# Kernel optimization log

Measured on AMD Instinct MI355X. Metric: run time of the kernel, lower is better.

## Reference

```python
import jax, jax.numpy as jnp
import numpy as np

EPS = 1e-5


def _batchnorm(x, gamma, beta):
    # training-mode batch norm over the node axis, per feature channel
    mean = jnp.mean(x, axis=0)
    var = jnp.var(x, axis=0)  # biased variance, as torch uses for normalization
    return (x - mean) * jax.lax.rsqrt(var + EPS) * gamma + beta


def _gcn_conv(h, W, b, src, dst, norm, n_nodes):
    # h: [N, Fin] -> [N, Fout]; D^{-1/2}(A+I)D^{-1/2} (h W) + b
    h = h @ W                                   # [N, Fout]
    msgs = h[src] * norm[:, None]               # [E+N, Fout] gathered, normalized
    out = jax.ops.segment_sum(msgs, dst, num_segments=n_nodes)
    return out + b


def setup_inputs() -> dict:
    key = jax.random.key(0)
    ks = jax.random.split(key, 8)
    N, F, E, H = 50000, 512, 800000, 256
    inp = {
        "x": jax.random.normal(ks[0], (N, F), jnp.float32),
        "edge_index": jax.random.randint(ks[1], (2, E), 0, N, jnp.int64),
        "gamma1": jnp.ones((F,), jnp.float32),
        "beta1": jnp.zeros((F,), jnp.float32),
        "W1": jax.random.normal(ks[2], (F, H), jnp.float32) * (1.0 / np.sqrt(F)),
        "b1": jnp.zeros((H,), jnp.float32),
        "W2": jax.random.normal(ks[3], (H, H), jnp.float32) * (1.0 / np.sqrt(H)),
        "b2": jnp.zeros((H,), jnp.float32),
        "W3": jax.random.normal(ks[4], (H, H), jnp.float32) * (1.0 / np.sqrt(H)),
        "b3": jnp.zeros((H,), jnp.float32),
        "W4": jax.random.normal(ks[5], (H, H), jnp.float32) * (1.0 / np.sqrt(H)),
        "b4": jnp.zeros((H,), jnp.float32),
        "gamma2": jnp.ones((H,), jnp.float32),
        "beta2": jnp.zeros((H,), jnp.float32),
        "Wd": jax.random.normal(ks[6], (H, 5), jnp.float32) * (1.0 / np.sqrt(H)),
        "bd": jnp.zeros((5,), jnp.float32),
    }
    return inp


def reference(x, edge_index, gamma1, beta1, W1, b1, W2, b2, W3, b3, W4, b4,
              gamma2, beta2, Wd, bd):
    N = x.shape[0]
    loops = jnp.arange(N, dtype=edge_index.dtype)
    src = jnp.concatenate([edge_index[0], loops])
    dst = jnp.concatenate([edge_index[1], loops])
    deg = jax.ops.segment_sum(jnp.ones_like(src, dtype=x.dtype), dst, num_segments=N)
    dinv = jax.lax.rsqrt(deg)                    # deg >= 1 due to self-loops
    norm = dinv[src] * dinv[dst]                 # [E+N]

    h = _batchnorm(x, gamma1, beta1)
    h = _gcn_conv(h, W1, b1, src, dst, norm, N)
    h = _gcn_conv(h, W2, b2, src, dst, norm, N)
    h = _gcn_conv(h, W3, b3, src, dst, norm, N)
    h = _gcn_conv(h, W4, b4, src, dst, norm, N)
    h = _batchnorm(h, gamma2, beta2)
    # Flatten(start_dim=1) is identity on [N, 256]
    return jax.nn.sigmoid(h @ Wd + bd)           # [N, 5]
```

## Files before the change

kernel.cpp:

```cpp
#include <hip/hip_runtime.h>
#include <math.h>

#define BN_EPS 1e-5f

typedef float floatx4 __attribute__((ext_vector_type(4)));
typedef short shortx4 __attribute__((ext_vector_type(4)));
typedef short shortx8 __attribute__((ext_vector_type(8)));
typedef __bf16 bf16x8 __attribute__((ext_vector_type(8)));

__device__ __forceinline__ unsigned short f2b(float f) {
    unsigned int u = __builtin_bit_cast(unsigned int, f);
    u += 0x7fffu + ((u >> 16) & 1u);
    return (unsigned short)(u >> 16);
}
__device__ __forceinline__ float b2f(unsigned short s) {
    unsigned int u = ((unsigned int)s) << 16;
    return __builtin_bit_cast(float, u);
}
__device__ __forceinline__ float b2f_s(short s) { return b2f((unsigned short)s); }

__global__ __launch_bounds__(256)
void k_detect(const unsigned int* __restrict__ ei, int n_check, int* __restrict__ flag) {
    __shared__ int any;
    if (threadIdx.x == 0) any = 0;
    __syncthreads();
    for (int i = threadIdx.x; i < n_check; i += 256) {
        if (ei[2 * i + 1] != 0u) any = 1;
    }
    __syncthreads();
    if (threadIdx.x == 0) *flag = any;
}

__global__ __launch_bounds__(256)
void k_convert(const void* __restrict__ ei_raw, const int* __restrict__ flag,
               int* __restrict__ src, int* __restrict__ dst, int E) {
    int e = blockIdx.x * 256 + threadIdx.x;
    if (e >= E) return;
    if (*flag) {
        const int* a = (const int*)ei_raw;
        src[e] = a[e];
        dst[e] = a[E + e];
    } else {
        const long long* a = (const long long*)ei_raw;
        src[e] = (int)a[e];
        dst[e] = (int)a[E + e];
    }
}

__global__ __launch_bounds__(256)
void k_count(const int* __restrict__ dst, int* __restrict__ cnt, int E) {
    int e = blockIdx.x * 256 + threadIdx.x;
    if (e < E) atomicAdd(&cnt[dst[e]], 1);
}

__global__ __launch_bounds__(1024)
void k_scan_sum(const int* __restrict__ cnt, int* __restrict__ bsum, int N) {
    __shared__ int s[1024];
    int i = blockIdx.x * 1024 + threadIdx.x;
    s[threadIdx.x] = (i < N) ? cnt[i] : 0;
    __syncthreads();
    for (int off = 512; off > 0; off >>= 1) {
        if (threadIdx.x < off) s[threadIdx.x] += s[threadIdx.x + off];
        __syncthreads();
    }
    if (threadIdx.x == 0) bsum[blockIdx.x] = s[0];
}

__global__ __launch_bounds__(1024)
void k_scan_part(int* __restrict__ bsum, int nb) {
    __shared__ int s[1024];
    int t = threadIdx.x;
    int v = (t < nb) ? bsum[t] : 0;
    s[t] = v;
    __syncthreads();
    for (int off = 1; off < 1024; off <<= 1) {
        int tmp = (t >= off) ? s[t - off] : 0;
        __syncthreads();
        s[t] += tmp;
        __syncthreads();
    }
    if (t < nb) bsum[t] = s[t] - v;
}

__global__ __launch_bounds__(1024)
void k_scan_final(const int* __restrict__ cnt, const int* __restrict__ bsum,
                  int* __restrict__ row_ptr, int* __restrict__ cursor,
                  float* __restrict__ dinv, int N) {
    __shared__ int s[1024];
    int b = blockIdx.x, t = threadIdx.x;
    int i = b * 1024 + t;
    int v = (i < N) ? cnt[i] : 0;
    s[t] = v;
    __syncthreads();
    for (int off = 1; off < 1024; off <<= 1) {
        int tmp = (t >= off) ? s[t - off] : 0;
        __syncthreads();
        s[t] += tmp;
        __syncthreads();
    }
    if (i < N) {
        int excl = bsum[b] + s[t] - v;
        row_ptr[i] = excl;
        cursor[i]  = excl;
        dinv[i] = rsqrtf((float)(v + 1));
        if (i == N - 1) row_ptr[N] = excl + v;
    }
}

__global__ __launch_bounds__(256)
void k_fill(const int* __restrict__ src, const int* __restrict__ dst,
            int* __restrict__ cursor, const float* __restrict__ dinv,
            int2* __restrict__ csr_sw, int E) {
    int e = blockIdx.x * 256 + threadIdx.x;
    if (e >= E) return;
    int s = src[e], d = dst[e];
    int p = atomicAdd(&cursor[d], 1);
    float w = dinv[s] * dinv[d];
    csr_sw[p] = make_int2(s, __builtin_bit_cast(int, w));
}

__global__ __launch_bounds__(256)
void k_bnstats(const float* __restrict__ x, float* __restrict__ sum, float* __restrict__ sumsq,
               int N, int F) {
    __shared__ float ls[512], lq[512];
    int q   = F >> 2;
    int t   = threadIdx.x;
    int cq  = t % q;
    int ro  = t / q;
    int rpp = 256 / q;
    int step = gridDim.x * rpp;
    float s0 = 0.f, s1 = 0.f, s2 = 0.f, s3 = 0.f;
    float q0 = 0.f, q1 = 0.f, q2 = 0.f, q3 = 0.f;
    for (int r = blockIdx.x * rpp + ro; r < N; r += 2 * step) {
        float4 v = *(const float4*)&x[(size_t)r * F + cq * 4];
        int r2 = r + step;
        if (r2 < N) {
            float4 u = *(const float4*)&x[(size_t)r2 * F + cq * 4];
            s0 += u.x; s1 += u.y; s2 += u.z; s3 += u.w;
            q0 += u.x * u.x; q1 += u.y * u.y; q2 += u.z * u.z; q3 += u.w * u.w;
        }
        s0 += v.x; s1 += v.y; s2 += v.z; s3 += v.w;
        q0 += v.x * v.x; q1 += v.y * v.y; q2 += v.z * v.z; q3 += v.w * v.w;
    }
    for (int c = t; c < F; c += 256) { ls[c] = 0.f; lq[c] = 0.f; }
    __syncthreads();
    atomicAdd(&ls[cq * 4 + 0], s0); atomicAdd(&ls[cq * 4 + 1], s1);
    atomicAdd(&ls[cq * 4 + 2], s2); atomicAdd(&ls[cq * 4 + 3], s3);
    atomicAdd(&lq[cq * 4 + 0], q0); atomicAdd(&lq[cq * 4 + 1], q1);
    atomicAdd(&lq[cq * 4 + 2], q2); atomicAdd(&lq[cq * 4 + 3], q3);
    __syncthreads();
    for (int c = t; c < F; c += 256) {
        atomicAdd(&sum[c],   ls[c]);
        atomicAdd(&sumsq[c], lq[c]);
    }
}

__global__ __launch_bounds__(256)
void k_bnstats_b(const unsigned short* __restrict__ x, float* __restrict__ sum,
                 float* __restrict__ sumsq, int N, int H) {
    __shared__ float ls[256], lq[256];
    int t  = threadIdx.x;
    int cg = t & 31;
    int ro = t >> 5;
    int step = gridDim.x * 8;
    float s[8], q[8];
    #pragma unroll
    for (int j = 0; j < 8; ++j) { s[j] = 0.f; q[j] = 0.f; }
    for (int r = blockIdx.x * 8 + ro; r < N; r += step) {
        shortx8 v = *(const shortx8*)&x[(size_t)r * H + cg * 8];
        #pragma unroll
        for (int j = 0; j < 8; ++j) {
            float f = b2f_s(v[j]);
            s[j] += f; q[j] += f * f;
        }
    }
    ls[t] = 0.f; lq[t] = 0.f;
    __syncthreads();
    #pragma unroll
    for (int j = 0; j < 8; ++j) {
        atomicAdd(&ls[cg * 8 + j], s[j]);
        atomicAdd(&lq[cg * 8 + j], q[j]);
    }
    __syncthreads();
    atomicAdd(&sum[t],   ls[t]);
    atomicAdd(&sumsq[t], lq[t]);
}

__global__ __launch_bounds__(256)
void k_bnfin(const float* __restrict__ sum, const float* __restrict__ sumsq,
             const float* __restrict__ gamma, const float* __restrict__ beta,
             float* __restrict__ a, float* __restrict__ b, int N, int F) {
    int c = blockIdx.x * 256 + threadIdx.x;
    if (c >= F) return;
    float m   = sum[c] / (float)N;
    float var = sumsq[c] / (float)N - m * m;
    float rs  = rsqrtf(var + BN_EPS);
    float aa  = gamma[c] * rs;
    a[c] = aa;
    b[c] = beta[c] - m * aa;
}

__global__ __launch_bounds__(256)
void k_cast_bn(const float* __restrict__ x, const float* __restrict__ a, const float* __restrict__ b,
               unsigned short* __restrict__ xb, int N, int F, int Mpad) {
    int i = blockIdx.x * 256 + threadIdx.x;
    int total = Mpad * (F / 8);
    if (i >= total) return;
    int row = i / (F / 8);
    int col = (i % (F / 8)) * 8;
    shortx8 v;
    if (row < N) {
        float4 x0 = *(const float4*)&x[(size_t)row * F + col];
        float4 x1 = *(const float4*)&x[(size_t)row * F + col + 4];
        float4 a0 = *(const float4*)&a[col];
        float4 a1 = *(const float4*)&a[col + 4];
        float4 b0 = *(const float4*)&b[col];
        float4 b1 = *(const float4*)&b[col + 4];
        v[0] = (short)f2b(x0.x * a0.x + b0.x);
        v[1] = (short)f2b(x0.y * a0.y + b0.y);
        v[2] = (short)f2b(x0.z * a0.z + b0.z);
        v[3] = (short)f2b(x0.w * a0.w + b0.w);
        v[4] = (short)f2b(x1.x * a1.x + b1.x);
        v[5] = (short)f2b(x1.y * a1.y + b1.y);
        v[6] = (short)f2b(x1.z * a1.z + b1.z);
        v[7] = (short)f2b(x1.w * a1.w + b1.w);
    } else {
        #pragma unroll
        for (int j = 0; j < 8; ++j) v[j] = 0;
    }
    *(shortx8*)&xb[(size_t)row * F + col] = v;
}

__global__ __launch_bounds__(256)
void k_castWT4(const float* __restrict__ W1, const float* __restrict__ W2,
               const float* __restrict__ W3, const float* __restrict__ W4,
               unsigned short* __restrict__ T1, unsigned short* __restrict__ T2,
               unsigned short* __restrict__ T3, unsigned short* __restrict__ T4,
               int F, int H) {
    int i = blockIdx.x * 256 + threadIdx.x;
    int n1 = F * H, n2 = H * H;
    const float* W; unsigned short* T; int K; int j;
    if (i < n1)               { W = W1; T = T1; K = F; j = i; }
    else if (i < n1 + n2)     { W = W2; T = T2; K = H; j = i - n1; }
    else if (i < n1 + 2 * n2) { W = W3; T = T3; K = H; j = i - n1 - n2; }
    else if (i < n1 + 3 * n2) { W = W4; T = T4; K = H; j = i - n1 - 2 * n2; }
    else return;
    int n = j / K, k = j % K;
    T[j] = f2b(W[(size_t)k * H + n]);
}

__device__ __forceinline__ void glds16(const void* g, void* l) {
    __builtin_amdgcn_global_load_lds(
        (const __attribute__((address_space(1))) unsigned int*)g,
        (__attribute__((address_space(3))) unsigned int*)l, 16, 0, 0);
}

__global__ __launch_bounds__(256)
void k_gemm_bf16(const unsigned short* __restrict__ A, const unsigned short* __restrict__ Bt,
                 unsigned short* __restrict__ C, int K, int NC) {
    __shared__ unsigned short As[128 * 32];
    __shared__ unsigned short Bs[128 * 32];
    int tid  = threadIdx.x;
    int wave = tid >> 6, lane = tid & 63;
    int row0 = blockIdx.x * 128;
    int col0 = blockIdx.y * 128;
    int wr = (wave & 1) * 64;
    int wc = (wave >> 1) * 64;

    floatx4 acc[4][4];
    #pragma unroll
    for (int i = 0; i < 4; i++)
        #pragma unroll
        for (int j = 0; j < 4; j++) acc[i][j] = (floatx4){0.f, 0.f, 0.f, 0.f};

    int cA = tid * 16;
    int cB = cA + 4096;
    const char* Ab = (const char*)A;
    const char* Bb = (const char*)Bt;
    size_t a_off0 = (size_t)(row0 + (cA >> 6)) * K * 2 + (cA & 63);
    size_t a_off1 = (size_t)(row0 + (cB >> 6)) * K * 2 + (cB & 63);
    size_t b_off0 = (size_t)(col0 + (cA >> 6)) * K * 2 + (cA & 63);
    size_t b_off1 = (size_t)(col0 + (cB >> 6)) * K * 2 + (cB & 63);

    int lm  = lane & 15;
    int lk8 = (lane >> 4) * 8;

    for (int ks = 0; ks < K; ks += 32) {
        size_t koff = (size_t)ks * 2;
        glds16(Ab + a_off0 + koff, (char*)As + cA);
        glds16(Ab + a_off1 + koff, (char*)As + cA + 4096);
        glds16(Bb + b_off0 + koff, (char*)Bs + cA);
        glds16(Bb + b_off1 + koff, (char*)Bs + cA + 4096);
        __syncthreads();

        bf16x8 af[4], bfr[4];
        #pragma unroll
        for (int i = 0; i < 4; i++) {
            shortx8 s = *(const shortx8*)&As[(wr + i * 16 + lm) * 32 + lk8];
            af[i] = __builtin_bit_cast(bf16x8, s);
        }
        #pragma unroll
        for (int j = 0; j < 4; j++) {
            shortx8 s = *(const shortx8*)&Bs[(wc + j * 16 + lm) * 32 + lk8];
            bfr[j] = __builtin_bit_cast(bf16x8, s);
        }
        #pragma unroll
        for (int i = 0; i < 4; i++)
            #pragma unroll
            for (int j = 0; j < 4; j++)
                acc[i][j] = __builtin_amdgcn_mfma_f32_16x16x32_bf16(af[i], bfr[j], acc[i][j], 0, 0, 0);
        __syncthreads();
    }

    int crow = row0 + wr + (lane >> 4) * 4;
    int ccol = col0 + wc + lm;
    #pragma unroll
    for (int i = 0; i < 4; i++)
        #pragma unroll
        for (int j = 0; j < 4; j++)
            #pragma unroll
            for (int r = 0; r < 4; r++)
                C[(size_t)(crow + i * 16 + r) * NC + ccol + j * 16] = f2b(acc[i][j][r]);
}

__global__ __launch_bounds__(256)
void k_agg(const unsigned short* __restrict__ hin, unsigned short* __restrict__ hout,
           const int* __restrict__ row_ptr, const int2* __restrict__ csr_sw,
           const float* __restrict__ dinv, const float* __restrict__ bias, int N) {
    const int H = 256;
    int node = blockIdx.x * 4 + (threadIdx.x >> 6);
    if (node >= N) return;
    int lane = threadIdx.x & 63;
    int half = lane >> 5;
    int f = (lane & 31) * 8;
    float acc[8];
    float di = dinv[node];
    if (half == 0) {
        shortx8 hv = *(const shortx8*)&hin[(size_t)node * H + f];
        float sl = di * di;
        #pragma unroll
        for (int j = 0; j < 8; ++j) acc[j] = b2f_s(hv[j]) * sl;
    } else {
        #pragma unroll
        for (int j = 0; j < 8; ++j) acc[j] = 0.f;
    }
    int e0 = row_ptr[node], e1 = row_ptr[node + 1];
    int e = e0;
    for (; e + 8 <= e1; e += 8) {
        int2 p0 = csr_sw[e + 0 + half];
        int2 p1 = csr_sw[e + 2 + half];
        int2 p2 = csr_sw[e + 4 + half];
        int2 p3 = csr_sw[e + 6 + half];
        shortx8 r0 = *(const shortx8*)&hin[(size_t)p0.x * H + f];
        shortx8 r1 = *(const shortx8*)&hin[(size_t)p1.x * H + f];
        shortx8 r2 = *(const shortx8*)&hin[(size_t)p2.x * H + f];
        shortx8 r3 = *(const shortx8*)&hin[(size_t)p3.x * H + f];
        float w0 = __builtin_bit_cast(float, p0.y);
        float w1 = __builtin_bit_cast(float, p1.y);
        float w2 = __builtin_bit_cast(float, p2.y);
        float w3 = __builtin_bit_cast(float, p3.y);
        #pragma unroll
        for (int j = 0; j < 8; ++j)
            acc[j] += w0 * b2f_s(r0[j]) + w1 * b2f_s(r1[j])
                    + w2 * b2f_s(r2[j]) + w3 * b2f_s(r3[j]);
    }
    for (; e < e1; e += 2) {
        int idx = e + half;
        bool valid = idx < e1;
        int2 pr = csr_sw[valid ? idx : e];
        float w = valid ? __builtin_bit_cast(float, pr.y) : 0.f;
        shortx8 r = *(const shortx8*)&hin[(size_t)pr.x * H + f];
        #pragma unroll
        for (int j = 0; j < 8; ++j) acc[j] += w * b2f_s(r[j]);
    }
    #pragma unroll
    for (int j = 0; j < 8; ++j) acc[j] += __shfl_xor(acc[j], 32, 64);
    if (half == 0) {
        float4 bi0 = *(const float4*)&bias[f];
        float4 bi1 = *(const float4*)&bias[f + 4];
        shortx8 o;
        o[0] = (short)f2b(acc[0] + bi0.x);
        o[1] = (short)f2b(acc[1] + bi0.y);
        o[2] = (short)f2b(acc[2] + bi0.z);
        o[3] = (short)f2b(acc[3] + bi0.w);
        o[4] = (short)f2b(acc[4] + bi1.x);
        o[5] = (short)f2b(acc[5] + bi1.y);
        o[6] = (short)f2b(acc[6] + bi1.z);
        o[7] = (short)f2b(acc[7] + bi1.w);
        *(shortx8*)&hout[(size_t)node * H + f] = o;
    }
}

__global__ __launch_bounds__(256)
void k_head(const unsigned short* __restrict__ h, const float* __restrict__ a,
            const float* __restrict__ b, const float* __restrict__ Wd,
            const float* __restrict__ bd, float* __restrict__ out, int N) {
    int node = blockIdx.x * 4 + (threadIdx.x >> 6);
    if (node >= N) return;
    int lane = threadIdx.x & 63;
    int f = lane * 4;
    shortx4 hv = *(const shortx4*)&h[(size_t)node * 256 + f];
    float v0 = b2f_s(hv[0]) * a[f + 0] + b[f + 0];
    float v1 = b2f_s(hv[1]) * a[f + 1] + b[f + 1];
    float v2 = b2f_s(hv[2]) * a[f + 2] + b[f + 2];
    float v3 = b2f_s(hv[3]) * a[f + 3] + b[f + 3];
    float s[5];
    #pragma unroll
    for (int j = 0; j < 5; ++j) {
        s[j] = v0 * Wd[(f + 0) * 5 + j] + v1 * Wd[(f + 1) * 5 + j] +
               v2 * Wd[(f + 2) * 5 + j] + v3 * Wd[(f + 3) * 5 + j];
    }
    #pragma unroll
    for (int off = 32; off > 0; off >>= 1) {
        #pragma unroll
        for (int j = 0; j < 5; ++j) s[j] += __shfl_down(s[j], off, 64);
    }
    if (lane == 0) {
        #pragma unroll
        for (int j = 0; j < 5; ++j) {
            float z = s[j] + bd[j];
            out[(size_t)node * 5 + j] = 1.f / (1.f + expf(-z));
        }
    }
}

extern "C" void kernel_launch(void* const* d_in, const int* in_sizes, int n_in,
                              void* d_out, int out_size, void* d_ws, size_t ws_size,
                              hipStream_t stream) {
    const float* x      = (const float*)d_in[0];
    const void*  ei_raw = d_in[1];
    const float* gamma1 = (const float*)d_in[2];
    const float* beta1  = (const float*)d_in[3];
    const float* W1 = (const float*)d_in[4];
    const float* b1 = (const float*)d_in[5];
    const float* W2 = (const float*)d_in[6];
    const float* b2 = (const float*)d_in[7];
    const float* W3 = (const float*)d_in[8];
    const float* b3 = (const float*)d_in[9];
    const float* W4 = (const float*)d_in[10];
    const float* b4 = (const float*)d_in[11];
    const float* gamma2 = (const float*)d_in[12];
    const float* beta2  = (const float*)d_in[13];
    const float* Wd = (const float*)d_in[14];
    const float* bd = (const float*)d_in[15];

    const int F = in_sizes[2];
    const int N = in_sizes[0] / F;
    const int E = in_sizes[1] / 2;
    const int H = in_sizes[5];
    const int Mpad = ((N + 127) / 128) * 128;
    const int NB   = (N + 1023) / 1024;
    float* out = (float*)d_out;

    char* p = (char*)d_ws;
    auto alloc = [&](size_t bytes) {
        void* r = (void*)p;
        p += (bytes + 255) & ~(size_t)255;
        return r;
    };
    int*   flag    = (int*)  alloc(4);
    int*   srcA    = (int*)  alloc((size_t)E * 4);
    int*   dstA    = (int*)  alloc((size_t)E * 4);
    int*   cnt     = (int*)  alloc((size_t)N * 4);
    int*   row_ptr = (int*)  alloc(((size_t)N + 1) * 4);
    int*   cursor  = (int*)  alloc((size_t)N * 4);
    float* dinv    = (float*)alloc((size_t)N * 4);
    int2*  csr_sw  = (int2*) alloc((size_t)E * 8);
    int*   bsum    = (int*)  alloc((size_t)NB * 4);
    float* colsum  = (float*)alloc((size_t)F * 4);
    float* colsq   = (float*)alloc((size_t)F * 4);
    float* bna     = (float*)alloc((size_t)F * 4);
    float* bnb     = (float*)alloc((size_t)F * 4);
    unsigned short* W1t = (unsigned short*)alloc((size_t)F * H * 2);
    unsigned short* W2t = (unsigned short*)alloc((size_t)H * H * 2);
    unsigned short* W3t = (unsigned short*)alloc((size_t)H * H * 2);
    unsigned short* W4t = (unsigned short*)alloc((size_t)H * H * 2);
    unsigned short* xb  = (unsigned short*)alloc((size_t)Mpad * F * 2);
    unsigned short* hbA = (unsigned short*)alloc((size_t)Mpad * H * 2);
    unsigned short* hbB = (unsigned short*)alloc((size_t)Mpad * H * 2);

    hipMemsetAsync(cnt,    0, (size_t)N * 4, stream);
    hipMemsetAsync(colsum, 0, (size_t)F * 4, stream);
    hipMemsetAsync(colsq,  0, (size_t)F * 4, stream);

    int n_check = (E >= 2048) ? 2048 : E;
    k_detect<<<1, 256, 0, stream>>>((const unsigned int*)ei_raw, n_check, flag);
    k_convert<<<(E + 255) / 256, 256, 0, stream>>>(ei_raw, flag, srcA, dstA, E);
    k_count<<<(E + 255) / 256, 256, 0, stream>>>(dstA, cnt, E);
    k_scan_sum<<<NB, 1024, 0, stream>>>(cnt, bsum, N);
    k_scan_part<<<1, 1024, 0, stream>>>(bsum, NB);
    k_scan_final<<<NB, 1024, 0, stream>>>(cnt, bsum, row_ptr, cursor, dinv, N);
    k_fill<<<(E + 255) / 256, 256, 0, stream>>>(srcA, dstA, cursor, dinv, csr_sw, E);

    k_bnstats<<<1024, 256, 0, stream>>>(x, colsum, colsq, N, F);
    k_bnfin<<<(F + 255) / 256, 256, 0, stream>>>(colsum, colsq, gamma1, beta1, bna, bnb, N, F);
    k_cast_bn<<<(Mpad * (F / 8) + 255) / 256, 256, 0, stream>>>(x, bna, bnb, xb, N, F, Mpad);

    int tot = F * H + 3 * H * H;
    k_castWT4<<<(tot + 255) / 256, 256, 0, stream>>>(W1, W2, W3, W4, W1t, W2t, W3t, W4t, F, H);

    dim3 gg(Mpad / 128, H / 128);
    int aggb = (N + 3) / 4;
    k_gemm_bf16<<<gg, 256, 0, stream>>>(xb, W1t, hbA, F, H);
    k_agg<<<aggb, 256, 0, stream>>>(hbA, hbB, row_ptr, csr_sw, dinv, b1, N);
    k_gemm_bf16<<<gg, 256, 0, stream>>>(hbB, W2t, hbA, H, H);
    k_agg<<<aggb, 256, 0, stream>>>(hbA, hbB, row_ptr, csr_sw, dinv, b2, N);
    k_gemm_bf16<<<gg, 256, 0, stream>>>(hbB, W3t, hbA, H, H);
    k_agg<<<aggb, 256, 0, stream>>>(hbA, hbB, row_ptr, csr_sw, dinv, b3, N);
    k_gemm_bf16<<<gg, 256, 0, stream>>>(hbB, W4t, hbA, H, H);
    k_agg<<<aggb, 256, 0, stream>>>(hbA, hbB, row_ptr, csr_sw, dinv, b4, N);

    hipMemsetAsync(colsum, 0, (size_t)H * 4, stream);
    hipMemsetAsync(colsq,  0, (size_t)H * 4, stream);
    k_bnstats_b<<<512, 256, 0, stream>>>(hbB, colsum, colsq, N, H);
    k_bnfin<<<(H + 255) / 256, 256, 0, stream>>>(colsum, colsq, gamma2, beta2, bna, bnb, N, H);
    k_head<<<(N + 3) / 4, 256, 0, stream>>>(hbB, bna, bnb, Wd, bd, out, N);
}
```

Baseline: 712.9 us.

## Fold batchnorm affine into W1 and fuse stats with bf16 cast

The first batchnorm is folded algebraically into the first layer. The scale multiplies into the transposed W1, and the shift becomes a per-feature bias vector scaled by the row sum of aggregation weights inside the first aggregation. This lets the stats pass also write the raw bf16 copy of x, removing a second full read of the 100MB input. Edge conversion and degree counting are fused, and column-sum atomics are spread over replicated buffers to reduce contention. The trade-off is that bf16 rounding now happens on unnormalized x, which may change accuracy slightly.

Measured after the change: 693.4 us. 2.7% less time.

```diff
diff --git a/kernel.cpp b/kernel.cpp
--- a/kernel.cpp
+++ b/kernel.cpp
@@ -33,24 +33,20 @@
 
 __global__ __launch_bounds__(256)
 void k_convert(const void* __restrict__ ei_raw, const int* __restrict__ flag,
-               int* __restrict__ src, int* __restrict__ dst, int E) {
+               int* __restrict__ src, int* __restrict__ dst, int* __restrict__ cnt, int E) {
     int e = blockIdx.x * 256 + threadIdx.x;
     if (e >= E) return;
+    int s, d;
     if (*flag) {
         const int* a = (const int*)ei_raw;
-        src[e] = a[e];
-        dst[e] = a[E + e];
+        s = a[e]; d = a[E + e];
     } else {
         const long long* a = (const long long*)ei_raw;
-        src[e] = (int)a[e];
-        dst[e] = (int)a[E + e];
-    }
-}
-
-__global__ __launch_bounds__(256)
-void k_count(const int* __restrict__ dst, int* __restrict__ cnt, int E) {
-    int e = blockIdx.x * 256 + threadIdx.x;
-    if (e < E) atomicAdd(&cnt[dst[e]], 1);
+        s = (int)a[e]; d = (int)a[E + e];
+    }
+    src[e] = s;
+    dst[e] = d;
+    atomicAdd(&cnt[d], 1);
 }
 
 __global__ __launch_bounds__(1024)
@@ -120,8 +116,8 @@
 }
 
 __global__ __launch_bounds__(256)
-void k_bnstats(const float* __restrict__ x, float* __restrict__ sum, float* __restrict__ sumsq,
-               int N, int F) {
+void k_bnstats_cast(const float* __restrict__ x, unsigned short* __restrict__ xb,
+                    float* __restrict__ sum8, float* __restrict__ sumsq8, int N, int F) {
     __shared__ float ls[512], lq[512];
     int q   = F >> 2;
     int t   = threadIdx.x;
@@ -131,16 +127,42 @@
     int step = gridDim.x * rpp;
     float s0 = 0.f, s1 = 0.f, s2 = 0.f, s3 = 0.f;
     float q0 = 0.f, q1 = 0.f, q2 = 0.f, q3 = 0.f;
-    for (int r = blockIdx.x * rpp + ro; r < N; r += 2 * step) {
-        float4 v = *(const float4*)&x[(size_t)r * F + cq * 4];
-        int r2 = r + step;
-        if (r2 < N) {
-            float4 u = *(const float4*)&x[(size_t)r2 * F + cq * 4];
-            s0 += u.x; s1 += u.y; s2 += u.z; s3 += u.w;
-            q0 += u.x * u.x; q1 += u.y * u.y; q2 += u.z * u.z; q3 += u.w * u.w;
-        }
-        s0 += v.x; s1 += v.y; s2 += v.z; s3 += v.w;
-        q0 += v.x * v.x; q1 += v.y * v.y; q2 += v.z * v.z; q3 += v.w * v.w;
+    size_t colb = (size_t)cq * 4;
+    for (int r = blockIdx.x * rpp + ro; r < N; r += 4 * step) {
+        int rb = r + step, rc = r + 2 * step, rd = r + 3 * step;
+        bool ob = rb < N, oc = rc < N, od = rd < N;
+        float4 va = *(const float4*)&x[(size_t)r * F + colb];
+        float4 vb, vc, vd;
+        if (ob) vb = *(const float4*)&x[(size_t)rb * F + colb];
+        if (oc) vc = *(const float4*)&x[(size_t)rc * F + colb];
+        if (od) vd = *(const float4*)&x[(size_t)rd * F + colb];
+        shortx4 o;
+        o[0] = (short)f2b(va.x); o[1] = (short)f2b(va.y);
+        o[2] = (short)f2b(va.z); o[3] = (short)f2b(va.w);
+        *(shortx4*)&xb[(size_t)r * F + colb] = o;
+        s0 += va.x; s1 += va.y; s2 += va.z; s3 += va.w;
+        q0 += va.x * va.x; q1 += va.y * va.y; q2 += va.z * va.z; q3 += va.w * va.w;
+        if (ob) {
+            o[0] = (short)f2b(vb.x); o[1] = (short)f2b(vb.y);
+            o[2] = (short)f2b(vb.z); o[3] = (short)f2b(vb.w);
+            *(shortx4*)&xb[(size_t)rb * F + colb] = o;
+            s0 += vb.x; s1 += vb.y; s2 += vb.z; s3 += vb.w;
+            q0 += vb.x * vb.x; q1 += vb.y * vb.y; q2 += vb.z * vb.z; q3 += vb.w * vb.w;
+        }
+        if (oc) {
+            o[0] = (short)f2b(vc.x); o[1] = (short)f2b(vc.y);
+            o[2] = (short)f2b(vc.z); o[3] = (short)f2b(vc.w);
+            *(shortx4*)&xb[(size_t)rc * F + colb] = o;
+            s0 += vc.x; s1 += vc.y; s2 += vc.z; s3 += vc.w;
+            q0 += vc.x * vc.x; q1 += vc.y * vc.y; q2 += vc.z * vc.z; q3 += vc.w * vc.w;
+        }
+        if (od) {
+            o[0] = (short)f2b(vd.x); o[1] = (short)f2b(vd.y);
+            o[2] = (short)f2b(vd.z); o[3] = (short)f2b(vd.w);
+            *(shortx4*)&xb[(size_t)rd * F + colb] = o;
+            s0 += vd.x; s1 += vd.y; s2 += vd.z; s3 += vd.w;
+            q0 += vd.x * vd.x; q1 += vd.y * vd.y; q2 += vd.z * vd.z; q3 += vd.w * vd.w;
+        }
     }
     for (int c = t; c < F; c += 256) { ls[c] = 0.f; lq[c] = 0.f; }
     __syncthreads();
@@ -149,9 +171,10 @@
     atomicAdd(&lq[cq * 4 + 0], q0); atomicAdd(&lq[cq * 4 + 1], q1);
     atomicAdd(&lq[cq * 4 + 2], q2); atomicAdd(&lq[cq * 4 + 3], q3);
     __syncthreads();
+    int rep = (blockIdx.x & 7) * F;
     for (int c = t; c < F; c += 256) {
-        atomicAdd(&sum[c],   ls[c]);
-        atomicAdd(&sumsq[c], lq[c]);
+        atomicAdd(&sum8[rep + c],   ls[c]);
+        atomicAdd(&sumsq8[rep + c], lq[c]);
     }
 }
 
@@ -182,18 +205,21 @@
         atomicAdd(&lq[cg * 8 + j], q[j]);
     }
     __syncthreads();
-    atomicAdd(&sum[t],   ls[t]);
-    atomicAdd(&sumsq[t], lq[t]);
+    int rep = (blockIdx.x & 3) * H;
+    atomicAdd(&sum[rep + t],   ls[t]);
+    atomicAdd(&sumsq[rep + t], lq[t]);
 }
 
 __global__ __launch_bounds__(256)
 void k_bnfin(const float* __restrict__ sum, const float* __restrict__ sumsq,
              const float* __restrict__ gamma, const float* __restrict__ beta,
-             float* __restrict__ a, float* __restrict__ b, int N, int F) {
+             float* __restrict__ a, float* __restrict__ b, int N, int F, int nrep) {
     int c = blockIdx.x * 256 + threadIdx.x;
     if (c >= F) return;
-    float m   = sum[c] / (float)N;
-    float var = sumsq[c] / (float)N - m * m;
+    float s = 0.f, ss = 0.f;
+    for (int i = 0; i < nrep; ++i) { s += sum[i * F + c]; ss += sumsq[i * F + c]; }
+    float m   = s / (float)N;
+    float var = ss / (float)N - m * m;
     float rs  = rsqrtf(var + BN_EPS);
     float aa  = gamma[c] * rs;
     a[c] = aa;
@@ -201,52 +227,37 @@
 }
 
 __global__ __launch_bounds__(256)
-void k_cast_bn(const float* __restrict__ x, const float* __restrict__ a, const float* __restrict__ b,
-               unsigned short* __restrict__ xb, int N, int F, int Mpad) {
-    int i = blockIdx.x * 256 + threadIdx.x;
-    int total = Mpad * (F / 8);
-    if (i >= total) return;
-    int row = i / (F / 8);
-    int col = (i % (F / 8)) * 8;
-    shortx8 v;
-    if (row < N) {
-        float4 x0 = *(const float4*)&x[(size_t)row * F + col];
-        float4 x1 = *(const float4*)&x[(size_t)row * F + col + 4];
-        float4 a0 = *(const float4*)&a[col];
-        float4 a1 = *(const float4*)&a[col + 4];
-        float4 b0 = *(const float4*)&b[col];
-        float4 b1 = *(const float4*)&b[col + 4];
-        v[0] = (short)f2b(x0.x * a0.x + b0.x);
-        v[1] = (short)f2b(x0.y * a0.y + b0.y);
-        v[2] = (short)f2b(x0.z * a0.z + b0.z);
-        v[3] = (short)f2b(x0.w * a0.w + b0.w);
-        v[4] = (short)f2b(x1.x * a1.x + b1.x);
-        v[5] = (short)f2b(x1.y * a1.y + b1.y);
-        v[6] = (short)f2b(x1.z * a1.z + b1.z);
-        v[7] = (short)f2b(x1.w * a1.w + b1.w);
-    } else {
-        #pragma unroll
-        for (int j = 0; j < 8; ++j) v[j] = 0;
-    }
-    *(shortx8*)&xb[(size_t)row * F + col] = v;
-}
-
-__global__ __launch_bounds__(256)
 void k_castWT4(const float* __restrict__ W1, const float* __restrict__ W2,
                const float* __restrict__ W3, const float* __restrict__ W4,
                unsigned short* __restrict__ T1, unsigned short* __restrict__ T2,
                unsigned short* __restrict__ T3, unsigned short* __restrict__ T4,
-               int F, int H) {
+               const float* __restrict__ bna, int F, int H) {
     int i = blockIdx.x * 256 + threadIdx.x;
     int n1 = F * H, n2 = H * H;
-    const float* W; unsigned short* T; int K; int j;
-    if (i < n1)               { W = W1; T = T1; K = F; j = i; }
-    else if (i < n1 + n2)     { W = W2; T = T2; K = H; j = i - n1; }
-    else if (i < n1 + 2 * n2) { W = W3; T = T3; K = H; j = i - n1 - n2; }
-    else if (i < n1 + 3 * n2) { W = W4; T = T4; K = H; j = i - n1 - 2 * n2; }
+    if (i < n1) {
+        int n = i / F, k = i % F;
+        T1[i] = f2b(W1[(size_t)k * H + n] * bna[k]);
+        return;
+    }
+    const float* W; unsigned short* T; int j;
+    if (i < n1 + n2)          { W = W2; T = T2; j = i - n1; }
+    else if (i < n1 + 2 * n2) { W = W3; T = T3; j = i - n1 - n2; }
+    else if (i < n1 + 3 * n2) { W = W4; T = T4; j = i - n1 - 2 * n2; }
     else return;
-    int n = j / K, k = j % K;
+    int n = j / H, k = j % H;
     T[j] = f2b(W[(size_t)k * H + n]);
+}
+
+__global__ __launch_bounds__(256)
+void k_cvec(const float* __restrict__ W1, const float* __restrict__ bnb,
+            float* __restrict__ cvec, int F, int H) {
+    int j = threadIdx.x;
+    int kslice = F / 8;
+    int k0 = blockIdx.x * kslice;
+    float s = 0.f;
+    for (int k = k0; k < k0 + kslice; ++k)
+        s += bnb[k] * W1[(size_t)k * H + j];
+    atomicAdd(&cvec[j], s);
 }
 
 __device__ __forceinline__ void glds16(const void* g, void* l) {
@@ -326,7 +337,8 @@
 __global__ __launch_bounds__(256)
 void k_agg(const unsigned short* __restrict__ hin, unsigned short* __restrict__ hout,
            const int* __restrict__ row_ptr, const int2* __restrict__ csr_sw,
-           const float* __restrict__ dinv, const float* __restrict__ bias, int N) {
+           const float* __restrict__ dinv, const float* __restrict__ bias,
+           const float* __restrict__ cvec, int N) {
     const int H = 256;
     int node = blockIdx.x * 4 + (threadIdx.x >> 6);
     if (node >= N) return;
@@ -334,13 +346,16 @@
     int half = lane >> 5;
     int f = (lane & 31) * 8;
     float acc[8];
+    float ws;
     float di = dinv[node];
     if (half == 0) {
         shortx8 hv = *(const shortx8*)&hin[(size_t)node * H + f];
         float sl = di * di;
+        ws = sl;
         #pragma unroll
         for (int j = 0; j < 8; ++j) acc[j] = b2f_s(hv[j]) * sl;
     } else {
+        ws = 0.f;
         #pragma unroll
         for (int j = 0; j < 8; ++j) acc[j] = 0.f;
     }
@@ -359,6 +374,7 @@
         float w1 = __builtin_bit_cast(float, p1.y);
         float w2 = __builtin_bit_cast(float, p2.y);
         float w3 = __builtin_bit_cast(float, p3.y);
+        ws += (w0 + w1) + (w2 + w3);
         #pragma unroll
         for (int j = 0; j < 8; ++j)
             acc[j] += w0 * b2f_s(r0[j]) + w1 * b2f_s(r1[j])
@@ -370,14 +386,24 @@
         int2 pr = csr_sw[valid ? idx : e];
         float w = valid ? __builtin_bit_cast(float, pr.y) : 0.f;
         shortx8 r = *(const shortx8*)&hin[(size_t)pr.x * H + f];
+        ws += w;
         #pragma unroll
         for (int j = 0; j < 8; ++j) acc[j] += w * b2f_s(r[j]);
     }
     #pragma unroll
     for (int j = 0; j < 8; ++j) acc[j] += __shfl_xor(acc[j], 32, 64);
+    ws += __shfl_xor(ws, 32, 64);
     if (half == 0) {
         float4 bi0 = *(const float4*)&bias[f];
         float4 bi1 = *(const float4*)&bias[f + 4];
+        if (cvec) {
+            float4 c0 = *(const float4*)&cvec[f];
+            float4 c1 = *(const float4*)&cvec[f + 4];
+            bi0.x += ws * c0.x; bi0.y += ws * c0.y;
+            bi0.z += ws * c0.z; bi0.w += ws * c0.w;
+            bi1.x += ws * c1.x; bi1.y += ws * c1.y;
+            bi1.z += ws * c1.z; bi1.w += ws * c1.w;
+        }
         shortx8 o;
         o[0] = (short)f2b(acc[0] + bi0.x);
         o[1] = (short)f2b(acc[1] + bi0.y);
@@ -461,14 +487,19 @@
     int*   flag    = (int*)  alloc(4);
     int*   srcA    = (int*)  alloc((size_t)E * 4);
     int*   dstA    = (int*)  alloc((size_t)E * 4);
+    char*  zstart  = p;
     int*   cnt     = (int*)  alloc((size_t)N * 4);
+    float* colsum8 = (float*)alloc((size_t)8 * F * 4);
+    float* colsq8  = (float*)alloc((size_t)8 * F * 4);
+    float* colsum2 = (float*)alloc((size_t)4 * H * 4);
+    float* colsq2  = (float*)alloc((size_t)4 * H * 4);
+    float* cvec    = (float*)alloc((size_t)H * 4);
+    size_t zbytes  = (size_t)(p - zstart);
     int*   row_ptr = (int*)  alloc(((size_t)N + 1) * 4);
     int*   cursor  = (int*)  alloc((size_t)N * 4);
     float* dinv    = (float*)alloc((size_t)N * 4);
     int2*  csr_sw  = (int2*) alloc((size_t)E * 8);
     int*   bsum    = (int*)  alloc((size_t)NB * 4);
-    float* colsum  = (float*)alloc((size_t)F * 4);
-    float* colsq   = (float*)alloc((size_t)F * 4);
     float* bna     = (float*)alloc((size_t)F * 4);
     float* bnb     = (float*)alloc((size_t)F * 4);
     unsigned short* W1t = (unsigned short*)alloc((size_t)F * H * 2);
@@ -479,40 +510,36 @@
     unsigned short* hbA = (unsigned short*)alloc((size_t)Mpad * H * 2);
     unsigned short* hbB = (unsigned short*)alloc((size_t)Mpad * H * 2);
 
-    hipMemsetAsync(cnt,    0, (size_t)N * 4, stream);
-    hipMemsetAsync(colsum, 0, (size_t)F * 4, stream);
-    hipMemsetAsync(colsq,  0, (size_t)F * 4, stream);
+    hipMemsetAsync(zstart, 0, zbytes, stream);
+    hipMemsetAsync(xb + (size_t)N * F, 0, (size_t)(Mpad - N) * F * 2, stream);
 
     int n_check = (E >= 2048) ? 2048 : E;
     k_detect<<<1, 256, 0, stream>>>((const unsigned int*)ei_raw, n_check, flag);
-    k_convert<<<(E + 255) / 256, 256, 0, stream>>>(ei_raw, flag, srcA, dstA, E);
-    k_count<<<(E + 255) / 256, 256, 0, stream>>>(dstA, cnt, E);
+    k_convert<<<(E + 255) / 256, 256, 0, stream>>>(ei_raw, flag, srcA, dstA, cnt, E);
     k_scan_sum<<<NB, 1024, 0, stream>>>(cnt, bsum, N);
     k_scan_part<<<1, 1024, 0, stream>>>(bsum, NB);
     k_scan_final<<<NB, 1024, 0, stream>>>(cnt, bsum, row_ptr, cursor, dinv, N);
     k_fill<<<(E + 255) / 256, 256, 0, stream>>>(srcA, dstA, cursor, dinv, csr_sw, E);
 
-    k_bnstats<<<1024, 256, 0, stream>>>(x, colsum, colsq, N, F);
-    k_bnfin<<<(F + 255) / 256, 256, 0, stream>>>(colsum, colsq, gamma1, beta1, bna, bnb, N, F);
-    k_cast_bn<<<(Mpad * (F / 8) + 255) / 256, 256, 0, stream>>>(x, bna, bnb, xb, N, F, Mpad);
+    k_bnstats_cast<<<2048, 256, 0, stream>>>(x, xb, colsum8, colsq8, N, F);
+    k_bnfin<<<(F + 255) / 256, 256, 0, stream>>>(colsum8, colsq8, gamma1, beta1, bna, bnb, N, F, 8);
 
     int tot = F * H + 3 * H * H;
-    k_castWT4<<<(tot + 255) / 256, 256, 0, stream>>>(W1, W2, W3, W4, W1t, W2t, W3t, W4t, F, H);
+    k_castWT4<<<(tot + 255) / 256, 256, 0, stream>>>(W1, W2, W3, W4, W1t, W2t, W3t, W4t, bna, F, H);
+    k_cvec<<<8, 256, 0, stream>>>(W1, bnb, cvec, F, H);
 
     dim3 gg(Mpad / 128, H / 128);
     int aggb = (N + 3) / 4;
     k_gemm_bf16<<<gg, 256, 0, stream>>>(xb, W1t, hbA, F, H);
-    k_agg<<<aggb, 256, 0, stream>>>(hbA, hbB, row_ptr, csr_sw, dinv, b1, N);
+    k_agg<<<aggb, 256, 0, stream>>>(hbA, hbB, row_ptr, csr_sw, dinv, b1, cvec, N);
     k_gemm_bf16<<<gg, 256, 0, stream>>>(hbB, W2t, hbA, H, H);
-    k_agg<<<aggb, 256, 0, stream>>>(hbA, hbB, row_ptr, csr_sw, dinv, b2, N);
+    k_agg<<<aggb, 256, 0, stream>>>(hbA, hbB, row_ptr, csr_sw, dinv, b2, nullptr, N);
     k_gemm_bf16<<<gg, 256, 0, stream>>>(hbB, W3t, hbA, H, H);
-    k_agg<<<aggb, 256, 0, stream>>>(hbA, hbB, row_ptr, csr_sw, dinv, b3, N);
+    k_agg<<<aggb, 256, 0, stream>>>(hbA, hbB, row_ptr, csr_sw, dinv, b3, nullptr, N);
     k_gemm_bf16<<<gg, 256, 0, stream>>>(hbB, W4t, hbA, H, H);
-    k_agg<<<aggb, 256, 0, stream>>>(hbA, hbB, row_ptr, csr_sw, dinv, b4, N);
-
-    hipMemsetAsync(colsum, 0, (size_t)H * 4, stream);
-    hipMemsetAsync(colsq,  0, (size_t)H * 4, stream);
-    k_bnstats_b<<<512, 256, 0, stream>>>(hbB, colsum, colsq, N, H);
-    k_bnfin<<<(H + 255) / 256, 256, 0, stream>>>(colsum, colsq, gamma2, beta2, bna, bnb, N, H);
+    k_agg<<<aggb, 256, 0, stream>>>(hbA, hbB, row_ptr, csr_sw, dinv, b4, nullptr, N);
+
+    k_bnstats_b<<<1024, 256, 0, stream>>>(hbB, colsum2, colsq2, N, H);
+    k_bnfin<<<(H + 255) / 256, 256, 0, stream>>>(colsum2, colsq2, gamma2, beta2, bna, bnb, N, H, 4);
     k_head<<<(N + 3) / 4, 256, 0, stream>>>(hbB, bna, bnb, Wd, bd, out, N);
 }
```
